# Optimization experiments

Hardware: AMD Instinct MI355X
Metric: run time of the kernel (lower is better)

## Reference

```python
import jax, jax.numpy as jnp
import numpy as np


def setup_inputs() -> dict:
    key = jax.random.key(0)
    ks = jax.random.split(key, 9)
    B, Chsi, Cmsi, Cout, H, W = 2, 128, 64, 128, 80, 80
    return {
        "z_hsi": jax.random.normal(ks[0], (B, Chsi, H, W), dtype=jnp.float32),
        "z_msi": jax.random.normal(ks[1], (B, Cmsi, H, W), dtype=jnp.float32),
        "Wq": jax.random.normal(ks[2], (Cout, Chsi), dtype=jnp.float32) * 0.05,
        "bq": jax.random.normal(ks[3], (Cout,), dtype=jnp.float32) * 0.05,
        "Wk": jax.random.normal(ks[4], (Cout, Cmsi), dtype=jnp.float32) * 0.05,
        "bk": jax.random.normal(ks[5], (Cout,), dtype=jnp.float32) * 0.05,
        "Wv": jax.random.normal(ks[6], (Cout, Cmsi), dtype=jnp.float32) * 0.05,
        "bv": jax.random.normal(ks[7], (Cout,), dtype=jnp.float32) * 0.05,
        "gamma": jax.random.normal(ks[8], (1,), dtype=jnp.float32),
    }


def reference(z_hsi, z_msi, Wq, bq, Wk, bk, Wv, bv, gamma):
    B, C, H, W = z_hsi.shape
    N = H * W
    # 1x1 convs are per-pixel channel mixes
    q = jnp.einsum('bchw,oc->bohw', z_hsi, Wq) + bq[None, :, None, None]  # (B,O,H,W)
    k = jnp.einsum('bchw,oc->bohw', z_msi, Wk) + bk[None, :, None, None]
    v = jnp.einsum('bchw,oc->bohw', z_msi, Wv) + bv[None, :, None, None]
    q = q.reshape(B, -1, N)  # (B,O,N)
    k = k.reshape(B, -1, N)
    v = v.reshape(B, -1, N)
    # energy[b,i,j] = sum_o q[b,o,i] * k[b,o,j]  (unscaled, as in source)
    energy = jnp.einsum('boi,boj->bij', q, k)  # (B,N,N)
    attn = jax.nn.softmax(energy, axis=-1)
    # out[b,o,i] = sum_j v[b,o,j] * attn[b,i,j]
    out = jnp.einsum('boj,bij->boi', v, attn).reshape(B, -1, H, W)
    return gamma * out + z_hsi
```

## Files before the change

### kernel.cpp

```cpp
#include <hip/hip_runtime.h>
#include <hip/hip_bf16.h>
#include <hip/hip_fp16.h>

#define B_    2
#define N_    6400
#define CD_   128
#define CM_   64
#define SEG_  5
#define JSEG_ (N_ / SEG_)
#define JT_   64
#define NJT_  (JSEG_ / JT_)
#define NIT_  50

typedef __attribute__((ext_vector_type(8)))  short bf16x8;
typedef __attribute__((ext_vector_type(16))) float f32x16;
typedef __attribute__((ext_vector_type(2)))  __fp16 f16x2;

static __device__ __forceinline__ unsigned pack2bf(float a, float b) {
    union { float f; unsigned u; } x, y; x.f = a; y.f = b;
    return __builtin_amdgcn_perm(y.u + 0x8000u, x.u + 0x8000u, 0x07060302u);
}

static __device__ __forceinline__ unsigned cvtpk_bf16(float a, float b) {
    unsigned r;
    asm("v_cvt_pk_bf16_f32 %0, %1, %2" : "=v"(r) : "v"(a), "v"(b));
    return r;
}

__global__ __launch_bounds__(256, 4)
void proj2(const float* __restrict__ zh, const float* __restrict__ zm,
           const float* __restrict__ Wq, const float* __restrict__ bq,
           const float* __restrict__ Wk, const float* __restrict__ bk,
           const float* __restrict__ Wv, const float* __restrict__ bv,
           short* __restrict__ qb, short* __restrict__ kb, short* __restrict__ vb)
{
    __shared__ float zt[128 * 68];
    const int tid = threadIdx.x;
    int bid = blockIdx.x;
    const int qmode = bid < 400;
    if (!qmode) bid -= 400;
    const int b  = bid / 200;
    const int r  = bid % 200;
    const int i0 = (r >> 1) * 64;
    const int o0 = (r & 1) * 64;
    const int ig = tid & 15, og = tid >> 4;
    const int il = ig * 4;

    if (qmode) {
        const float* zsrc = zh + (size_t)b * CD_ * N_ + i0;
#pragma unroll
        for (int rep = 0; rep < 8; ++rep) {
            int idx = tid + rep * 256;
            int c = idx >> 4, f = idx & 15;
            *(float4*)&zt[c * 68 + f * 4] = *(const float4*)&zsrc[(size_t)c * N_ + f * 4];
        }
        __syncthreads();
        const float* wr0 = Wq + (size_t)(o0 + og * 4 + 0) * CD_;
        const float* wr1 = Wq + (size_t)(o0 + og * 4 + 1) * CD_;
        const float* wr2 = Wq + (size_t)(o0 + og * 4 + 2) * CD_;
        const float* wr3 = Wq + (size_t)(o0 + og * 4 + 3) * CD_;
        float acc[4][4];
#pragma unroll
        for (int oi = 0; oi < 4; ++oi) {
            float bb = bq[o0 + og * 4 + oi];
#pragma unroll
            for (int ri = 0; ri < 4; ++ri) acc[ri][oi] = bb;
        }
        for (int c4 = 0; c4 < 32; ++c4) {
            float4 w0 = *(const float4*)&wr0[c4 * 4];
            float4 w1 = *(const float4*)&wr1[c4 * 4];
            float4 w2 = *(const float4*)&wr2[c4 * 4];
            float4 w3 = *(const float4*)&wr3[c4 * 4];
            float ww[4][4] = {{w0.x,w1.x,w2.x,w3.x},{w0.y,w1.y,w2.y,w3.y},
                              {w0.z,w1.z,w2.z,w3.z},{w0.w,w1.w,w2.w,w3.w}};
#pragma unroll
            for (int cc = 0; cc < 4; ++cc) {
                float4 zr = *(float4*)&zt[(c4 * 4 + cc) * 68 + il];
                float zz[4] = {zr.x, zr.y, zr.z, zr.w};
#pragma unroll
                for (int ri = 0; ri < 4; ++ri)
#pragma unroll
                    for (int oi = 0; oi < 4; ++oi)
                        acc[ri][oi] = fmaf(zz[ri], ww[cc][oi], acc[ri][oi]);
            }
        }
#pragma unroll
        for (int ri = 0; ri < 4; ++ri) {
            uint2 pk = make_uint2(pack2bf(acc[ri][0], acc[ri][1]),
                                  pack2bf(acc[ri][2], acc[ri][3]));
            *(uint2*)&qb[((size_t)b * N_ + i0 + il + ri) * CD_ + o0 + og * 4] = pk;
        }
    } else {
        const float* zsrc = zm + (size_t)b * CM_ * N_ + i0;
#pragma unroll
        for (int rep = 0; rep < 4; ++rep) {
            int idx = tid + rep * 256;
            int c = idx >> 4, f = idx & 15;
            *(float4*)&zt[c * 68 + f * 4] = *(const float4*)&zsrc[(size_t)c * N_ + f * 4];
        }
        __syncthreads();
        const float* kr0 = Wk + (size_t)(o0 + og * 4 + 0) * CM_;
        const float* kr1 = Wk + (size_t)(o0 + og * 4 + 1) * CM_;
        const float* kr2 = Wk + (size_t)(o0 + og * 4 + 2) * CM_;
        const float* kr3 = Wk + (size_t)(o0 + og * 4 + 3) * CM_;
        const float* vr0 = Wv + (size_t)(o0 + og * 4 + 0) * CM_;
        const float* vr1 = Wv + (size_t)(o0 + og * 4 + 1) * CM_;
        const float* vr2 = Wv + (size_t)(o0 + og * 4 + 2) * CM_;
        const float* vr3 = Wv + (size_t)(o0 + og * 4 + 3) * CM_;
        float ak[4][4], av[4][4];
#pragma unroll
        for (int oi = 0; oi < 4; ++oi) {
            float bk0 = bk[o0 + og * 4 + oi], bv0 = bv[o0 + og * 4 + oi];
#pragma unroll
            for (int ri = 0; ri < 4; ++ri) { ak[ri][oi] = bk0; av[ri][oi] = bv0; }
        }
        for (int c4 = 0; c4 < 16; ++c4) {
            float4 k0 = *(const float4*)&kr0[c4 * 4];
            float4 k1 = *(const float4*)&kr1[c4 * 4];
            float4 k2 = *(const float4*)&kr2[c4 * 4];
            float4 k3 = *(const float4*)&kr3[c4 * 4];
            float4 v0 = *(const float4*)&vr0[c4 * 4];
            float4 v1 = *(const float4*)&vr1[c4 * 4];
            float4 v2 = *(const float4*)&vr2[c4 * 4];
            float4 v3 = *(const float4*)&vr3[c4 * 4];
            float kk[4][4] = {{k0.x,k1.x,k2.x,k3.x},{k0.y,k1.y,k2.y,k3.y},
                              {k0.z,k1.z,k2.z,k3.z},{k0.w,k1.w,k2.w,k3.w}};
            float vv[4][4] = {{v0.x,v1.x,v2.x,v3.x},{v0.y,v1.y,v2.y,v3.y},
                              {v0.z,v1.z,v2.z,v3.z},{v0.w,v1.w,v2.w,v3.w}};
#pragma unroll
            for (int cc = 0; cc < 4; ++cc) {
                float4 zr = *(float4*)&zt[(c4 * 4 + cc) * 68 + il];
                float zz[4] = {zr.x, zr.y, zr.z, zr.w};
#pragma unroll
                for (int ri = 0; ri < 4; ++ri)
#pragma unroll
                    for (int oi = 0; oi < 4; ++oi) {
                        ak[ri][oi] = fmaf(zz[ri], kk[cc][oi], ak[ri][oi]);
                        av[ri][oi] = fmaf(zz[ri], vv[cc][oi], av[ri][oi]);
                    }
            }
        }
#pragma unroll
        for (int ri = 0; ri < 4; ++ri) {
            uint2 pk = make_uint2(pack2bf(ak[ri][0], ak[ri][1]),
                                  pack2bf(ak[ri][2], ak[ri][3]));
            *(uint2*)&kb[((size_t)b * N_ + i0 + il + ri) * CD_ + o0 + og * 4] = pk;
        }
        const size_t vbase = (size_t)b * CD_ * N_;
#pragma unroll
        for (int oi = 0; oi < 4; ++oi) {
            uint2 pk = make_uint2(pack2bf(av[0][oi], av[1][oi]),
                                  pack2bf(av[2][oi], av[3][oi]));
            *(uint2*)&vb[vbase + (size_t)(o0 + og * 4 + oi) * N_ + i0 + il] = pk;
        }
    }
}

__global__ __launch_bounds__(256, 2)
void flash6(const short* __restrict__ qb, const short* __restrict__ kb,
            const short* __restrict__ vb, __fp16* __restrict__ Op,
            float* __restrict__ ml)
{
    __shared__ short Ks[2][64 * 128];
    __shared__ short Vs[2][128 * 64];

    const int tid   = threadIdx.x;
    const int wid   = tid >> 6;
    const int lane  = tid & 63;
    const int m5    = lane & 31;
    const int h     = lane >> 5;
    const int m15   = m5 & 15;
    const int l4r   = lane >> 4;
    const int pc    = (lane & 15) ^ l4r;

    const int vrow = lane >> 3;
    const int vc8  = (lane & 7) ^ (vrow & 7);
    const int voff = vrow * (N_ * 2) + vc8 * 16;

    const int bid = blockIdx.x;
    const int s   = bid % SEG_;
    const int bIt = bid / SEG_;
    const int b   = bIt >= NIT_ ? 1 : 0;
    const int it  = bIt - b * NIT_;
    const int i0  = it * 128;
    const int jbase = s * JSEG_;

    const short* qbp = qb + (size_t)b * N_ * CD_;
    const short* kbp = kb + (size_t)b * N_ * CD_;
    const char*  vstage = (const char*)(vb + (size_t)b * CD_ * N_) + voff;

    const int irow = i0 + wid * 32 + m5;
    bf16x8 qf[8];
#pragma unroll
    for (int kw = 0; kw < 8; ++kw)
        qf[kw] = *(const bf16x8*)&qbp[(size_t)irow * CD_ + kw * 16 + h * 8];

    f32x16 acc[4];
#pragma unroll
    for (int os = 0; os < 4; ++os)
#pragma unroll
        for (int r2 = 0; r2 < 16; ++r2) acc[os][r2] = 0.f;
    float lrun = 0.f;

#pragma unroll
    for (int tt = 0; tt < 4; ++tt) {
        int t = wid * 4 + tt;
        int st = (4 * t) & 15;
        const char* g = (const char*)kbp + (size_t)(jbase + 4 * t + l4r) * 256
                        + ((pc ^ st) << 4);
        __builtin_amdgcn_global_load_lds(
            (const __attribute__((address_space(1))) void*)g,
            (__attribute__((address_space(3))) void*)&Ks[0][t * 512], 16, 0, 0);
    }
#pragma unroll
    for (int tt = 0; tt < 4; ++tt) {
        int t = wid * 4 + tt;
        const char* g = vstage + (size_t)(t * 8) * (N_ * 2) + (size_t)jbase * 2;
        __builtin_amdgcn_global_load_lds(
            (const __attribute__((address_space(1))) void*)g,
            (__attribute__((address_space(3))) void*)&Vs[0][t * 512], 16, 0, 0);
    }
    __syncthreads();

    for (int jti = 0; jti < NJT_; ++jti) {
        const int jt  = jbase + jti * JT_;
        const int cur = jti & 1;
        if (jti + 1 < NJT_) {
            const int jn = jt + JT_;
#pragma unroll
            for (int tt = 0; tt < 4; ++tt) {
                int t = wid * 4 + tt;
                int st = (4 * t) & 15;
                const char* g = (const char*)kbp + (size_t)(jn + 4 * t + l4r) * 256
                                + ((pc ^ st) << 4);
                __builtin_amdgcn_global_load_lds(
                    (const __attribute__((address_space(1))) void*)g,
                    (__attribute__((address_space(3))) void*)&Ks[1 - cur][t * 512], 16, 0, 0);
            }
#pragma unroll
            for (int tt = 0; tt < 4; ++tt) {
                int t = wid * 4 + tt;
                const char* g = vstage + (size_t)(t * 8) * (N_ * 2) + (size_t)jn * 2;
                __builtin_amdgcn_global_load_lds(
                    (const __attribute__((address_space(1))) void*)g,
                    (__attribute__((address_space(3))) void*)&Vs[1 - cur][t * 512], 16, 0, 0);
            }
        }

        unsigned fr[4][4];
#pragma unroll
        for (int jc = 0; jc < 2; ++jc) {
            f32x16 sacc;
#pragma unroll
            for (int r2 = 0; r2 < 16; ++r2) sacc[r2] = 0.f;
            __builtin_amdgcn_s_setprio(1);
#pragma unroll
            for (int kw = 0; kw < 8; ++kw) {
                int c16 = (2 * kw + h) ^ m15;
                bf16x8 kf = *(const bf16x8*)&Ks[cur][(jc * 32 + m5) * 128 + c16 * 8];
                sacc = __builtin_amdgcn_mfma_f32_32x32x16_bf16(kf, qf[kw], sacc, 0, 0, 0);
            }
            __builtin_amdgcn_s_setprio(0);
            unsigned pk[8];
#pragma unroll
            for (int p = 0; p < 8; ++p) {
                float e0 = __expf(sacc[2 * p]     - 25.f);
                float e1 = __expf(sacc[2 * p + 1] - 25.f);
                lrun += e0 + e1;
                pk[p] = cvtpk_bf16(e0, e1);
            }
#pragma unroll
            for (int X = 0; X < 2; ++X) {
                auto r0 = __builtin_amdgcn_permlane32_swap(
                              pk[4 * X],     pk[4 * X + 2], false, false);
                auto r1 = __builtin_amdgcn_permlane32_swap(
                              pk[4 * X + 1], pk[4 * X + 3], false, false);
                fr[2 * jc + X][0] = (unsigned)r0[0];
                fr[2 * jc + X][1] = (unsigned)r1[0];
                fr[2 * jc + X][2] = (unsigned)r0[1];
                fr[2 * jc + X][3] = (unsigned)r1[1];
            }
        }
        __builtin_amdgcn_s_setprio(1);
#pragma unroll
        for (int kc = 0; kc < 4; ++kc) {
            union { unsigned u[4]; bf16x8 v; } pf;
#pragma unroll
            for (int u = 0; u < 4; ++u) pf.u[u] = fr[kc][u];
#pragma unroll
            for (int os = 0; os < 4; ++os) {
                int o = os * 32 + m5;
                int q = (kc * 2 + h) ^ (m5 & 7);
                bf16x8 vf = *(const bf16x8*)&Vs[cur][o * 64 + q * 8];
                acc[os] = __builtin_amdgcn_mfma_f32_32x32x16_bf16(vf, pf.v, acc[os], 0, 0, 0);
            }
        }
        __builtin_amdgcn_s_setprio(0);
        __syncthreads();
    }

    float lt = lrun + __shfl_xor(lrun, 32);
    if (h == 0) ml[((size_t)bIt * SEG_ + s) * 128 + wid * 32 + m5] = lt;
    const float linv = 1.0f / lt;

    float* Of = (float*)&Ks[0][0];
    __fp16* opb = Op + ((size_t)bIt * SEG_ + s) * (128 * CD_);
#pragma unroll
    for (int r = 0; r < 2; ++r) {
        __syncthreads();
        if ((wid >> 1) == r) {
            const int il_ = (wid & 1) * 32 + m5;
#pragma unroll
            for (int os = 0; os < 4; ++os) {
#pragma unroll
                for (int g = 0; g < 4; ++g) {
                    int q = os * 8 + g * 2 + h;
                    int p = q ^ m5;
                    *(float4*)&Of[il_ * 128 + p * 4] =
                        make_float4(acc[os][4 * g] * linv, acc[os][4 * g + 1] * linv,
                                    acc[os][4 * g + 2] * linv, acc[os][4 * g + 3] * linv);
                }
            }
        }
        __syncthreads();
#pragma unroll
        for (int u = 0; u < 8; ++u) {
            int G = u * 256 + tid;
            int i = G >> 5;
            int q = tid & 31;
            int p = q ^ (i & 31);
            float4 t = *(float4*)&Of[i * 128 + p * 4];
            union { f16x2 h2[2]; uint2 u2; } cv;
            cv.h2[0] = __builtin_amdgcn_cvt_pkrtz(t.x, t.y);
            cv.h2[1] = __builtin_amdgcn_cvt_pkrtz(t.z, t.w);
            *(uint2*)&opb[(size_t)r * 64 * CD_ + (size_t)G * 4] = cv.u2;
        }
    }
}

__global__ __launch_bounds__(256, 4)
void combine3(const __fp16* __restrict__ Op, const float* __restrict__ ml,
              const float* __restrict__ z_hsi, const float* __restrict__ gamma,
              float* __restrict__ out)
{
    __shared__ float T[CD_ * 36];
    __shared__ float wbuf[SEG_][32];
    const int tid = threadIdx.x;
    const int blk = blockIdx.x;
    const int bIt = blk >> 2;
    const int rq  = (blk & 3) * 32;
    const int b   = bIt / NIT_;
    const int it  = bIt % NIT_;
    const int i0  = it * 128 + rq;
    const float g = gamma[0];

    if (tid < 32) {
        float l[SEG_];
        float den = 0.f;
#pragma unroll
        for (int s2 = 0; s2 < SEG_; ++s2) {
            l[s2] = ml[((size_t)bIt * SEG_ + s2) * 128 + rq + tid];
            den += l[s2];
        }
        const float gd = g / den;
#pragma unroll
        for (int s2 = 0; s2 < SEG_; ++s2)
            wbuf[s2][tid] = l[s2] * gd;
    }
    __syncthreads();
    {
        const int i  = tid >> 3;
        const int oc = (tid & 7) * 4;
        float w[SEG_];
#pragma unroll
        for (int s2 = 0; s2 < SEG_; ++s2) w[s2] = wbuf[s2][i];
        const __fp16* base = Op + ((size_t)bIt * SEG_ * 128 + rq + i) * CD_ + oc;
#pragma unroll
        for (int c4 = 0; c4 < 4; ++c4) {
            float ax = 0.f, ay = 0.f, az = 0.f, aw = 0.f;
#pragma unroll
            for (int s2 = 0; s2 < SEG_; ++s2) {
                union { uint2 u2; f16x2 h2[2]; } raw;
                raw.u2 = *(const uint2*)&base[(size_t)s2 * 128 * CD_ + c4 * 32];
                ax = fmaf((float)raw.h2[0][0], w[s2], ax);
                ay = fmaf((float)raw.h2[0][1], w[s2], ay);
                az = fmaf((float)raw.h2[1][0], w[s2], az);
                aw = fmaf((float)raw.h2[1][1], w[s2], aw);
            }
            int o = oc + c4 * 32;
            T[(o + 0) * 36 + i] = ax;
            T[(o + 1) * 36 + i] = ay;
            T[(o + 2) * 36 + i] = az;
            T[(o + 3) * 36 + i] = aw;
        }
    }
    __syncthreads();
    {
        const int o = tid >> 1, ih = (tid & 1) * 16;
        const size_t gbase = ((size_t)b * CD_ + o) * N_ + i0 + ih;
#pragma unroll
        for (int rr = 0; rr < 4; ++rr) {
            float4 t  = *(float4*)&T[o * 36 + ih + rr * 4];
            float4 z4 = *(const float4*)&z_hsi[gbase + rr * 4];
            *(float4*)&out[gbase + rr * 4] =
                make_float4(t.x + z4.x, t.y + z4.y, t.z + z4.z, t.w + z4.w);
        }
    }
}

extern "C" void kernel_launch(void* const* d_in, const int* in_sizes, int n_in,
                              void* d_out, int out_size, void* d_ws, size_t ws_size,
                              hipStream_t stream) {
    const float* z_hsi = (const float*)d_in[0];
    const float* z_msi = (const float*)d_in[1];
    const float* Wq    = (const float*)d_in[2];
    const float* bq    = (const float*)d_in[3];
    const float* Wk    = (const float*)d_in[4];
    const float* bk    = (const float*)d_in[5];
    const float* Wv    = (const float*)d_in[6];
    const float* bv    = (const float*)d_in[7];
    const float* gamma = (const float*)d_in[8];
    float* out = (float*)d_out;

    const size_t nqb = (size_t)B_ * N_ * CD_;
    short* qb = (short*)d_ws;
    short* kb = qb + nqb;
    short* vb = kb + nqb;
    __fp16* Op = (__fp16*)(vb + nqb);
    float* ml = (float*)(Op + (size_t)100 * SEG_ * 128 * CD_);

    proj2<<<dim3(800), dim3(256), 0, stream>>>(z_hsi, z_msi, Wq, bq, Wk, bk, Wv, bv,
                                               qb, kb, vb);
    flash6<<<dim3(100 * SEG_), dim3(256), 0, stream>>>(qb, kb, vb, Op, ml);
    combine3<<<dim3(400), dim3(256), 0, stream>>>(Op, ml, z_hsi, gamma, out);
}
```

Measured before the change: 155.5 us.

## Fuse projection, flash attention and combine into one persistent kernel with grid barriers

Merges the three kernels into one persistent kernel of 500 blocks. Grid-wide atomic barriers separate the projection, attention and combine phases, and the projection work is looped over the resident blocks. It also folds log2(e) into q so the softmax can use exp2f with a pre-biased accumulator instead of __expf with a subtraction. This removes two kernel launch gaps and the tail effects between them, but relies on all 500 blocks being co-resident and adds a memset plus spin-wait barrier cost.

```diff
diff --git a/kernel.cpp b/kernel.cpp
--- a/kernel.cpp
+++ b/kernel.cpp
@@ -11,6 +11,8 @@
 #define JT_   64
 #define NJT_  (JSEG_ / JT_)
 #define NIT_  50
+#define GRID_ (NIT_ * 2 * SEG_)
+#define LOG2E_ 1.4426950408889634f
 
 typedef __attribute__((ext_vector_type(8)))  short bf16x8;
 typedef __attribute__((ext_vector_type(16))) float f32x16;
@@ -27,383 +29,400 @@
     return r;
 }
 
-__global__ __launch_bounds__(256, 4)
-void proj2(const float* __restrict__ zh, const float* __restrict__ zm,
+static __device__ __forceinline__ void gridbar(unsigned* bar) {
+    __syncthreads();
+    __threadfence();
+    if (threadIdx.x == 0) {
+        __hip_atomic_fetch_add(bar, 1u, __ATOMIC_RELEASE, __HIP_MEMORY_SCOPE_AGENT);
+        while (__hip_atomic_load(bar, __ATOMIC_ACQUIRE, __HIP_MEMORY_SCOPE_AGENT) < GRID_)
+            __builtin_amdgcn_s_sleep(1);
+    }
+    __syncthreads();
+    __threadfence();
+}
+
+__global__ __launch_bounds__(256, 2)
+void fused(const float* __restrict__ zh, const float* __restrict__ zm,
            const float* __restrict__ Wq, const float* __restrict__ bq,
            const float* __restrict__ Wk, const float* __restrict__ bk,
            const float* __restrict__ Wv, const float* __restrict__ bv,
-           short* __restrict__ qb, short* __restrict__ kb, short* __restrict__ vb)
+           short* __restrict__ qb, short* __restrict__ kb, short* __restrict__ vb,
+           __fp16* __restrict__ Op, float* __restrict__ ml,
+           const float* __restrict__ gamma, float* __restrict__ out,
+           unsigned* __restrict__ bar)
 {
-    __shared__ float zt[128 * 68];
+    __shared__ __align__(16) char smem[65536];
     const int tid = threadIdx.x;
-    int bid = blockIdx.x;
-    const int qmode = bid < 400;
-    if (!qmode) bid -= 400;
-    const int b  = bid / 200;
-    const int r  = bid % 200;
-    const int i0 = (r >> 1) * 64;
-    const int o0 = (r & 1) * 64;
-    const int ig = tid & 15, og = tid >> 4;
-    const int il = ig * 4;
-
-    if (qmode) {
-        const float* zsrc = zh + (size_t)b * CD_ * N_ + i0;
-#pragma unroll
-        for (int rep = 0; rep < 8; ++rep) {
-            int idx = tid + rep * 256;
-            int c = idx >> 4, f = idx & 15;
-            *(float4*)&zt[c * 68 + f * 4] = *(const float4*)&zsrc[(size_t)c * N_ + f * 4];
+
+    {
+        float* zt = (float*)smem;
+        const int ig = tid & 15, og = tid >> 4;
+        const int il = ig * 4;
+        for (int u = blockIdx.x; u < 800; u += GRID_) {
+            int ub = u;
+            const int qmode = ub < 400;
+            if (!qmode) ub -= 400;
+            const int b  = ub / 200;
+            const int r  = ub % 200;
+            const int i0 = (r >> 1) * 64;
+            const int o0 = (r & 1) * 64;
+
+            if (qmode) {
+                const float* zsrc = zh + (size_t)b * CD_ * N_ + i0;
+#pragma unroll
+                for (int rep = 0; rep < 8; ++rep) {
+                    int idx = tid + rep * 256;
+                    int c = idx >> 4, f = idx & 15;
+                    *(float4*)&zt[c * 68 + f * 4] = *(const float4*)&zsrc[(size_t)c * N_ + f * 4];
+                }
+                __syncthreads();
+                const float* wr0 = Wq + (size_t)(o0 + og * 4 + 0) * CD_;
+                const float* wr1 = Wq + (size_t)(o0 + og * 4 + 1) * CD_;
+                const float* wr2 = Wq + (size_t)(o0 + og * 4 + 2) * CD_;
+                const float* wr3 = Wq + (size_t)(o0 + og * 4 + 3) * CD_;
+                float acc[4][4];
+#pragma unroll
+                for (int oi = 0; oi < 4; ++oi) {
+                    float bb = bq[o0 + og * 4 + oi];
+#pragma unroll
+                    for (int ri = 0; ri < 4; ++ri) acc[ri][oi] = bb;
+                }
+                for (int c4 = 0; c4 < 32; ++c4) {
+                    float4 w0 = *(const float4*)&wr0[c4 * 4];
+                    float4 w1 = *(const float4*)&wr1[c4 * 4];
+                    float4 w2 = *(const float4*)&wr2[c4 * 4];
+                    float4 w3 = *(const float4*)&wr3[c4 * 4];
+                    float ww[4][4] = {{w0.x,w1.x,w2.x,w3.x},{w0.y,w1.y,w2.y,w3.y},
+                                      {w0.z,w1.z,w2.z,w3.z},{w0.w,w1.w,w2.w,w3.w}};
+#pragma unroll
+                    for (int cc = 0; cc < 4; ++cc) {
+                        float4 zr = *(float4*)&zt[(c4 * 4 + cc) * 68 + il];
+                        float zz[4] = {zr.x, zr.y, zr.z, zr.w};
+#pragma unroll
+                        for (int ri = 0; ri < 4; ++ri)
+#pragma unroll
+                            for (int oi = 0; oi < 4; ++oi)
+                                acc[ri][oi] = fmaf(zz[ri], ww[cc][oi], acc[ri][oi]);
+                    }
+                }
+#pragma unroll
+                for (int ri = 0; ri < 4; ++ri) {
+                    uint2 pk = make_uint2(
+                        pack2bf(acc[ri][0] * LOG2E_, acc[ri][1] * LOG2E_),
+                        pack2bf(acc[ri][2] * LOG2E_, acc[ri][3] * LOG2E_));
+                    *(uint2*)&qb[((size_t)b * N_ + i0 + il + ri) * CD_ + o0 + og * 4] = pk;
+                }
+            } else {
+                const float* zsrc = zm + (size_t)b * CM_ * N_ + i0;
+#pragma unroll
+                for (int rep = 0; rep < 4; ++rep) {
+                    int idx = tid + rep * 256;
+                    int c = idx >> 4, f = idx & 15;
+                    *(float4*)&zt[c * 68 + f * 4] = *(const float4*)&zsrc[(size_t)c * N_ + f * 4];
+                }
+                __syncthreads();
+                const float* kr0 = Wk + (size_t)(o0 + og * 4 + 0) * CM_;
+                const float* kr1 = Wk + (size_t)(o0 + og * 4 + 1) * CM_;
+                const float* kr2 = Wk + (size_t)(o0 + og * 4 + 2) * CM_;
+                const float* kr3 = Wk + (size_t)(o0 + og * 4 + 3) * CM_;
+                const float* vr0 = Wv + (size_t)(o0 + og * 4 + 0) * CM_;
+                const float* vr1 = Wv + (size_t)(o0 + og * 4 + 1) * CM_;
+                const float* vr2 = Wv + (size_t)(o0 + og * 4 + 2) * CM_;
+                const float* vr3 = Wv + (size_t)(o0 + og * 4 + 3) * CM_;
+                float ak[4][4], av[4][4];
+#pragma unroll
+                for (int oi = 0; oi < 4; ++oi) {
+                    float bk0 = bk[o0 + og * 4 + oi], bv0 = bv[o0 + og * 4 + oi];
+#pragma unroll
+                    for (int ri = 0; ri < 4; ++ri) { ak[ri][oi] = bk0; av[ri][oi] = bv0; }
+                }
+                for (int c4 = 0; c4 < 16; ++c4) {
+                    float4 k0 = *(const float4*)&kr0[c4 * 4];
+                    float4 k1 = *(const float4*)&kr1[c4 * 4];
+                    float4 k2 = *(const float4*)&kr2[c4 * 4];
+                    float4 k3 = *(const float4*)&kr3[c4 * 4];
+                    float4 v0 = *(const float4*)&vr0[c4 * 4];
+                    float4 v1 = *(const float4*)&vr1[c4 * 4];
+                    float4 v2 = *(const float4*)&vr2[c4 * 4];
+                    float4 v3 = *(const float4*)&vr3[c4 * 4];
+                    float kk[4][4] = {{k0.x,k1.x,k2.x,k3.x},{k0.y,k1.y,k2.y,k3.y},
+                                      {k0.z,k1.z,k2.z,k3.z},{k0.w,k1.w,k2.w,k3.w}};
+                    float vv[4][4] = {{v0.x,v1.x,v2.x,v3.x},{v0.y,v1.y,v2.y,v3.y},
+                                      {v0.z,v1.z,v2.z,v3.z},{v0.w,v1.w,v2.w,v3.w}};
+#pragma unroll
+                    for (int cc = 0; cc < 4; ++cc) {
+                        float4 zr = *(float4*)&zt[(c4 * 4 + cc) * 68 + il];
+                        float zz[4] = {zr.x, zr.y, zr.z, zr.w};
+#pragma unroll
+                        for (int ri = 0; ri < 4; ++ri)
+#pragma unroll
+                            for (int oi = 0; oi < 4; ++oi) {
+                                ak[ri][oi] = fmaf(zz[ri], kk[cc][oi], ak[ri][oi]);
+                                av[ri][oi] = fmaf(zz[ri], vv[cc][oi], av[ri][oi]);
+                            }
+                    }
+                }
+#pragma unroll
+                for (int ri = 0; ri < 4; ++ri) {
+                    uint2 pk = make_uint2(pack2bf(ak[ri][0], ak[ri][1]),
+                                          pack2bf(ak[ri][2], ak[ri][3]));
+                    *(uint2*)&kb[((size_t)b * N_ + i0 + il + ri) * CD_ + o0 + og * 4] = pk;
+                }
+                const size_t vbase = (size_t)b * CD_ * N_;
+#pragma unroll
+                for (int oi = 0; oi < 4; ++oi) {
+                    uint2 pk = make_uint2(pack2bf(av[0][oi], av[1][oi]),
+                                          pack2bf(av[2][oi], av[3][oi]));
+                    *(uint2*)&vb[vbase + (size_t)(o0 + og * 4 + oi) * N_ + i0 + il] = pk;
+                }
+            }
+            __syncthreads();
+        }
+    }
+
+    gridbar(&bar[0]);
+
+    {
+        short* Ks0 = (short*)smem;
+        short* Vs0 = (short*)(smem + 32768);
+
+        const int wid   = tid >> 6;
+        const int lane  = tid & 63;
+        const int m5    = lane & 31;
+        const int h     = lane >> 5;
+        const int m15   = m5 & 15;
+        const int l4r   = lane >> 4;
+        const int pc    = (lane & 15) ^ l4r;
+
+        const int vrow = lane >> 3;
+        const int vc8  = (lane & 7) ^ (vrow & 7);
+        const int voff = vrow * (N_ * 2) + vc8 * 16;
+
+        const int bid = blockIdx.x;
+        const int s   = bid % SEG_;
+        const int bIt = bid / SEG_;
+        const int b   = bIt >= NIT_ ? 1 : 0;
+        const int it  = bIt - b * NIT_;
+        const int i0  = it * 128;
+        const int jbase = s * JSEG_;
+
+        const short* qbp = qb + (size_t)b * N_ * CD_;
+        const short* kbp = kb + (size_t)b * N_ * CD_;
+        const char*  vstage = (const char*)(vb + (size_t)b * CD_ * N_) + voff;
+
+        const int irow = i0 + wid * 32 + m5;
+        bf16x8 qf[8];
+#pragma unroll
+        for (int kw = 0; kw < 8; ++kw)
+            qf[kw] = *(const bf16x8*)&qbp[(size_t)irow * CD_ + kw * 16 + h * 8];
+
+        f32x16 acc[4];
+#pragma unroll
+        for (int os = 0; os < 4; ++os)
+#pragma unroll
+            for (int r2 = 0; r2 < 16; ++r2) acc[os][r2] = 0.f;
+        float lrun = 0.f;
+
+#pragma unroll
+        for (int tt = 0; tt < 4; ++tt) {
+            int t = wid * 4 + tt;
+            int st = (4 * t) & 15;
+            const char* g = (const char*)kbp + (size_t)(jbase + 4 * t + l4r) * 256
+                            + ((pc ^ st) << 4);
+            __builtin_amdgcn_global_load_lds(
+                (const __attribute__((address_space(1))) void*)g,
+                (__attribute__((address_space(3))) void*)(Ks0 + t * 512), 16, 0, 0);
+        }
+#pragma unroll
+        for (int tt = 0; tt < 4; ++tt) {
+            int t = wid * 4 + tt;
+            const char* g = vstage + (size_t)(t * 8) * (N_ * 2) + (size_t)jbase * 2;
+            __builtin_amdgcn_global_load_lds(
+                (const __attribute__((address_space(1))) void*)g,
+                (__attribute__((address_space(3))) void*)(Vs0 + t * 512), 16, 0, 0);
         }
         __syncthreads();
-        const float* wr0 = Wq + (size_t)(o0 + og * 4 + 0) * CD_;
-        const float* wr1 = Wq + (size_t)(o0 + og * 4 + 1) * CD_;
-        const float* wr2 = Wq + (size_t)(o0 + og * 4 + 2) * CD_;
-        const float* wr3 = Wq + (size_t)(o0 + og * 4 + 3) * CD_;
-        float acc[4][4];
-#pragma unroll
-        for (int oi = 0; oi < 4; ++oi) {
-            float bb = bq[o0 + og * 4 + oi];
-#pragma unroll
-            for (int ri = 0; ri < 4; ++ri) acc[ri][oi] = bb;
-        }
-        for (int c4 = 0; c4 < 32; ++c4) {
-            float4 w0 = *(const float4*)&wr0[c4 * 4];
-            float4 w1 = *(const float4*)&wr1[c4 * 4];
-            float4 w2 = *(const float4*)&wr2[c4 * 4];
-            float4 w3 = *(const float4*)&wr3[c4 * 4];
-            float ww[4][4] = {{w0.x,w1.x,w2.x,w3.x},{w0.y,w1.y,w2.y,w3.y},
-                              {w0.z,w1.z,w2.z,w3.z},{w0.w,w1.w,w2.w,w3.w}};
-#pragma unroll
-            for (int cc = 0; cc < 4; ++cc) {
-                float4 zr = *(float4*)&zt[(c4 * 4 + cc) * 68 + il];
-                float zz[4] = {zr.x, zr.y, zr.z, zr.w};
-#pragma unroll
-                for (int ri = 0; ri < 4; ++ri)
-#pragma unroll
-                    for (int oi = 0; oi < 4; ++oi)
-                        acc[ri][oi] = fmaf(zz[ri], ww[cc][oi], acc[ri][oi]);
-            }
-        }
-#pragma unroll
-        for (int ri = 0; ri < 4; ++ri) {
-            uint2 pk = make_uint2(pack2bf(acc[ri][0], acc[ri][1]),
-                                  pack2bf(acc[ri][2], acc[ri][3]));
-            *(uint2*)&qb[((size_t)b * N_ + i0 + il + ri) * CD_ + o0 + og * 4] = pk;
-        }
-    } else {
-        const float* zsrc = zm + (size_t)b * CM_ * N_ + i0;
-#pragma unroll
-        for (int rep = 0; rep < 4; ++rep) {
-            int idx = tid + rep * 256;
-            int c = idx >> 4, f = idx & 15;
-            *(float4*)&zt[c * 68 + f * 4] = *(const float4*)&zsrc[(size_t)c * N_ + f * 4];
+
+        for (int jti = 0; jti < NJT_; ++jti) {
+            const int jt  = jbase + jti * JT_;
+            const int cur = jti & 1;
+            if (jti + 1 < NJT_) {
+                const int jn = jt + JT_;
+#pragma unroll
+                for (int tt = 0; tt < 4; ++tt) {
+                    int t = wid * 4 + tt;
+                    int st = (4 * t) & 15;
+                    const char* g = (const char*)kbp + (size_t)(jn + 4 * t + l4r) * 256
+                                    + ((pc ^ st) << 4);
+                    __builtin_amdgcn_global_load_lds(
+                        (const __attribute__((address_space(1))) void*)g,
+                        (__attribute__((address_space(3))) void*)(Ks0 + (1 - cur) * 8192 + t * 512), 16, 0, 0);
+                }
+#pragma unroll
+                for (int tt = 0; tt < 4; ++tt) {
+                    int t = wid * 4 + tt;
+                    const char* g = vstage + (size_t)(t * 8) * (N_ * 2) + (size_t)jn * 2;
+                    __builtin_amdgcn_global_load_lds(
+                        (const __attribute__((address_space(1))) void*)g,
+                        (__attribute__((address_space(3))) void*)(Vs0 + (1 - cur) * 8192 + t * 512), 16, 0, 0);
+                }
+            }
+
+            unsigned fr[4][4];
+#pragma unroll
+            for (int jc = 0; jc < 2; ++jc) {
+                f32x16 sacc;
+#pragma unroll
+                for (int r2 = 0; r2 < 16; ++r2) sacc[r2] = -36.067376022224085f;
+                __builtin_amdgcn_s_setprio(1);
+#pragma unroll
+                for (int kw = 0; kw < 8; ++kw) {
+                    int c16 = (2 * kw + h) ^ m15;
+                    bf16x8 kf = *(const bf16x8*)&Ks0[cur * 8192 + (jc * 32 + m5) * 128 + c16 * 8];
+                    sacc = __builtin_amdgcn_mfma_f32_32x32x16_bf16(kf, qf[kw], sacc, 0, 0, 0);
+                }
+                __builtin_amdgcn_s_setprio(0);
+                unsigned pk[8];
+#pragma unroll
+                for (int p = 0; p < 8; ++p) {
+                    float e0 = exp2f(sacc[2 * p]);
+                    float e1 = exp2f(sacc[2 * p + 1]);
+                    lrun += e0 + e1;
+                    pk[p] = cvtpk_bf16(e0, e1);
+                }
+#pragma unroll
+                for (int X = 0; X < 2; ++X) {
+                    auto r0 = __builtin_amdgcn_permlane32_swap(
+                                  pk[4 * X],     pk[4 * X + 2], false, false);
+                    auto r1 = __builtin_amdgcn_permlane32_swap(
+                                  pk[4 * X + 1], pk[4 * X + 3], false, false);
+                    fr[2 * jc + X][0] = (unsigned)r0[0];
+                    fr[2 * jc + X][1] = (unsigned)r1[0];
+                    fr[2 * jc + X][2] = (unsigned)r0[1];
+                    fr[2 * jc + X][3] = (unsigned)r1[1];
+                }
+            }
+            __builtin_amdgcn_s_setprio(1);
+#pragma unroll
+            for (int kc = 0; kc < 4; ++kc) {
+                union { unsigned u[4]; bf16x8 v; } pf;
+#pragma unroll
+                for (int u = 0; u < 4; ++u) pf.u[u] = fr[kc][u];
+#pragma unroll
+                for (int os = 0; os < 4; ++os) {
+                    int o = os * 32 + m5;
+                    int q = (kc * 2 + h) ^ (m5 & 7);
+                    bf16x8 vf = *(const bf16x8*)&Vs0[cur * 8192 + o * 64 + q * 8];
+                    acc[os] = __builtin_amdgcn_mfma_f32_32x32x16_bf16(vf, pf.v, acc[os], 0, 0, 0);
+                }
+            }
+            __builtin_amdgcn_s_setprio(0);
+            __syncthreads();
+        }
+
+        float lt = lrun + __shfl_xor(lrun, 32);
+        if (h == 0) ml[((size_t)bIt * SEG_ + s) * 128 + wid * 32 + m5] = lt;
+        const float linv = 1.0f / lt;
+
+        float* Of = (float*)smem;
+        __fp16* opb = Op + ((size_t)bIt * SEG_ + s) * (128 * CD_);
+#pragma unroll
+        for (int r = 0; r < 2; ++r) {
+            __syncthreads();
+            if ((wid >> 1) == r) {
+                const int il_ = (wid & 1) * 32 + m5;
+#pragma unroll
+                for (int os = 0; os < 4; ++os) {
+#pragma unroll
+                    for (int g = 0; g < 4; ++g) {
+                        int q = os * 8 + g * 2 + h;
+                        int p = q ^ m5;
+                        *(float4*)&Of[il_ * 128 + p * 4] =
+                            make_float4(acc[os][4 * g] * linv, acc[os][4 * g + 1] * linv,
+                                        acc[os][4 * g + 2] * linv, acc[os][4 * g + 3] * linv);
+                    }
+                }
+            }
+            __syncthreads();
+#pragma unroll
+            for (int u = 0; u < 8; ++u) {
+                int G = u * 256 + tid;
+                int i = G >> 5;
+                int q = tid & 31;
+                int p = q ^ (i & 31);
+                float4 t = *(float4*)&Of[i * 128 + p * 4];
+                union { f16x2 h2[2]; uint2 u2; } cv;
+                cv.h2[0] = __builtin_amdgcn_cvt_pkrtz(t.x, t.y);
+                cv.h2[1] = __builtin_amdgcn_cvt_pkrtz(t.z, t.w);
+                *(uint2*)&opb[(size_t)r * 64 * CD_ + (size_t)G * 4] = cv.u2;
+            }
+        }
+    }
+
+    gridbar(&bar[1]);
+
+    if (blockIdx.x < 400) {
+        float* T = (float*)smem;
+        float (*wbuf)[32] = (float(*)[32])(smem + 18944);
+        const int blk = blockIdx.x;
+        const int bIt = blk >> 2;
+        const int rq  = (blk & 3) * 32;
+        const int b   = bIt / NIT_;
+        const int it  = bIt % NIT_;
+        const int i0  = it * 128 + rq;
+        const float g = gamma[0];
+
+        if (tid < 32) {
+            float l[SEG_];
+            float den = 0.f;
+#pragma unroll
+            for (int s2 = 0; s2 < SEG_; ++s2) {
+                l[s2] = ml[((size_t)bIt * SEG_ + s2) * 128 + rq + tid];
+                den += l[s2];
+            }
+            const float gd = g / den;
+#pragma unroll
+            for (int s2 = 0; s2 < SEG_; ++s2)
+                wbuf[s2][tid] = l[s2] * gd;
         }
         __syncthreads();
-        const float* kr0 = Wk + (size_t)(o0 + og * 4 + 0) * CM_;
-        const float* kr1 = Wk + (size_t)(o0 + og * 4 + 1) * CM_;
-        const float* kr2 = Wk + (size_t)(o0 + og * 4 + 2) * CM_;
-        const float* kr3 = Wk + (size_t)(o0 + og * 4 + 3) * CM_;
-        const float* vr0 = Wv + (size_t)(o0 + og * 4 + 0) * CM_;
-        const float* vr1 = Wv + (size_t)(o0 + og * 4 + 1) * CM_;
-        const float* vr2 = Wv + (size_t)(o0 + og * 4 + 2) * CM_;
-        const float* vr3 = Wv + (size_t)(o0 + og * 4 + 3) * CM_;
-        float ak[4][4], av[4][4];
-#pragma unroll
-        for (int oi = 0; oi < 4; ++oi) {
-            float bk0 = bk[o0 + og * 4 + oi], bv0 = bv[o0 + og * 4 + oi];
-#pragma unroll
-            for (int ri = 0; ri < 4; ++ri) { ak[ri][oi] = bk0; av[ri][oi] = bv0; }
-        }
-        for (int c4 = 0; c4 < 16; ++c4) {
-            float4 k0 = *(const float4*)&kr0[c4 * 4];
-            float4 k1 = *(const float4*)&kr1[c4 * 4];
-            float4 k2 = *(const float4*)&kr2[c4 * 4];
-            float4 k3 = *(const float4*)&kr3[c4 * 4];
-            float4 v0 = *(const float4*)&vr0[c4 * 4];
-            float4 v1 = *(const float4*)&vr1[c4 * 4];
-            float4 v2 = *(const float4*)&vr2[c4 * 4];
-            float4 v3 = *(const float4*)&vr3[c4 * 4];
-            float kk[4][4] = {{k0.x,k1.x,k2.x,k3.x},{k0.y,k1.y,k2.y,k3.y},
-                              {k0.z,k1.z,k2.z,k3.z},{k0.w,k1.w,k2.w,k3.w}};
-            float vv[4][4] = {{v0.x,v1.x,v2.x,v3.x},{v0.y,v1.y,v2.y,v3.y},
-                              {v0.z,v1.z,v2.z,v3.z},{v0.w,v1.w,v2.w,v3.w}};
-#pragma unroll
-            for (int cc = 0; cc < 4; ++cc) {
-                float4 zr = *(float4*)&zt[(c4 * 4 + cc) * 68 + il];
-                float zz[4] = {zr.x, zr.y, zr.z, zr.w};
-#pragma unroll
-                for (int ri = 0; ri < 4; ++ri)
-#pragma unroll
-                    for (int oi = 0; oi < 4; ++oi) {
-                        ak[ri][oi] = fmaf(zz[ri], kk[cc][oi], ak[ri][oi]);
-                        av[ri][oi] = fmaf(zz[ri], vv[cc][oi], av[ri][oi]);
-                    }
-            }
-        }
-#pragma unroll
-        for (int ri = 0; ri < 4; ++ri) {
-            uint2 pk = make_uint2(pack2bf(ak[ri][0], ak[ri][1]),
-                                  pack2bf(ak[ri][2], ak[ri][3]));
-            *(uint2*)&kb[((size_t)b * N_ + i0 + il + ri) * CD_ + o0 + og * 4] = pk;
-        }
-        const size_t vbase = (size_t)b * CD_ * N_;
-#pragma unroll
-        for (int oi = 0; oi < 4; ++oi) {
-            uint2 pk = make_uint2(pack2bf(av[0][oi], av[1][oi]),
-                                  pack2bf(av[2][oi], av[3][oi]));
-            *(uint2*)&vb[vbase + (size_t)(o0 + og * 4 + oi) * N_ + i0 + il] = pk;
-        }
-    }
-}
-
-__global__ __launch_bounds__(256, 2)
-void flash6(const short* __restrict__ qb, const short* __restrict__ kb,
-            const short* __restrict__ vb, __fp16* __restrict__ Op,
-            float* __restrict__ ml)
-{
-    __shared__ short Ks[2][64 * 128];
-    __shared__ short Vs[2][128 * 64];
-
-    const int tid   = threadIdx.x;
-    const int wid   = tid >> 6;
-    const int lane  = tid & 63;
-    const int m5    = lane & 31;
-    const int h     = lane >> 5;
-    const int m15   = m5 & 15;
-    const int l4r   = lane >> 4;
-    const int pc    = (lane & 15) ^ l4r;
-
-    const int vrow = lane >> 3;
-    const int vc8  = (lane & 7) ^ (vrow & 7);
-    const int voff = vrow * (N_ * 2) + vc8 * 16;
-
-    const int bid = blockIdx.x;
-    const int s   = bid % SEG_;
-    const int bIt = bid / SEG_;
-    const int b   = bIt >= NIT_ ? 1 : 0;
-    const int it  = bIt - b * NIT_;
-    const int i0  = it * 128;
-    const int jbase = s * JSEG_;
-
-    const short* qbp = qb + (size_t)b * N_ * CD_;
-    const short* kbp = kb + (size_t)b * N_ * CD_;
-    const char*  vstage = (const char*)(vb + (size_t)b * CD_ * N_) + voff;
-
-    const int irow = i0 + wid * 32 + m5;
-    bf16x8 qf[8];
-#pragma unroll
-    for (int kw = 0; kw < 8; ++kw)
-        qf[kw] = *(const bf16x8*)&qbp[(size_t)irow * CD_ + kw * 16 + h * 8];
-
-    f32x16 acc[4];
-#pragma unroll
-    for (int os = 0; os < 4; ++os)
-#pragma unroll
-        for (int r2 = 0; r2 < 16; ++r2) acc[os][r2] = 0.f;
-    float lrun = 0.f;
-
-#pragma unroll
-    for (int tt = 0; tt < 4; ++tt) {
-        int t = wid * 4 + tt;
-        int st = (4 * t) & 15;
-        const char* g = (const char*)kbp + (size_t)(jbase + 4 * t + l4r) * 256
-                        + ((pc ^ st) << 4);
-        __builtin_amdgcn_global_load_lds(
-            (const __attribute__((address_space(1))) void*)g,
-            (__attribute__((address_space(3))) void*)&Ks[0][t * 512], 16, 0, 0);
-    }
-#pragma unroll
-    for (int tt = 0; tt < 4; ++tt) {
-        int t = wid * 4 + tt;
-        const char* g = vstage + (size_t)(t * 8) * (N_ * 2) + (size_t)jbase * 2;
-        __builtin_amdgcn_global_load_lds(
-            (const __attribute__((address_space(1))) void*)g,
-            (__attribute__((address_space(3))) void*)&Vs[0][t * 512], 16, 0, 0);
-    }
-    __syncthreads();
-
-    for (int jti = 0; jti < NJT_; ++jti) {
-        const int jt  = jbase + jti * JT_;
-        const int cur = jti & 1;
-        if (jti + 1 < NJT_) {
-            const int jn = jt + JT_;
-#pragma unroll
-            for (int tt = 0; tt < 4; ++tt) {
-                int t = wid * 4 + tt;
-                int st = (4 * t) & 15;
-                const char* g = (const char*)kbp + (size_t)(jn + 4 * t + l4r) * 256
-                                + ((pc ^ st) << 4);
-                __builtin_amdgcn_global_load_lds(
-                    (const __attribute__((address_space(1))) void*)g,
-                    (__attribute__((address_space(3))) void*)&Ks[1 - cur][t * 512], 16, 0, 0);
-            }
-#pragma unroll
-            for (int tt = 0; tt < 4; ++tt) {
-                int t = wid * 4 + tt;
-                const char* g = vstage + (size_t)(t * 8) * (N_ * 2) + (size_t)jn * 2;
-                __builtin_amdgcn_global_load_lds(
-                    (const __attribute__((address_space(1))) void*)g,
-                    (__attribute__((address_space(3))) void*)&Vs[1 - cur][t * 512], 16, 0, 0);
-            }
-        }
-
-        unsigned fr[4][4];
-#pragma unroll
-        for (int jc = 0; jc < 2; ++jc) {
-            f32x16 sacc;
-#pragma unroll
-            for (int r2 = 0; r2 < 16; ++r2) sacc[r2] = 0.f;
-            __builtin_amdgcn_s_setprio(1);
-#pragma unroll
-            for (int kw = 0; kw < 8; ++kw) {
-                int c16 = (2 * kw + h) ^ m15;
-                bf16x8 kf = *(const bf16x8*)&Ks[cur][(jc * 32 + m5) * 128 + c16 * 8];
-                sacc = __builtin_amdgcn_mfma_f32_32x32x16_bf16(kf, qf[kw], sacc, 0, 0, 0);
-            }
-            __builtin_amdgcn_s_setprio(0);
-            unsigned pk[8];
-#pragma unroll
-            for (int p = 0; p < 8; ++p) {
-                float e0 = __expf(sacc[2 * p]     - 25.f);
-                float e1 = __expf(sacc[2 * p + 1] - 25.f);
-                lrun += e0 + e1;
-                pk[p] = cvtpk_bf16(e0, e1);
-            }
-#pragma unroll
-            for (int X = 0; X < 2; ++X) {
-                auto r0 = __builtin_amdgcn_permlane32_swap(
-                              pk[4 * X],     pk[4 * X + 2], false, false);
-                auto r1 = __builtin_amdgcn_permlane32_swap(
-                              pk[4 * X + 1], pk[4 * X + 3], false, false);
-                fr[2 * jc + X][0] = (unsigned)r0[0];
-                fr[2 * jc + X][1] = (unsigned)r1[0];
-                fr[2 * jc + X][2] = (unsigned)r0[1];
-                fr[2 * jc + X][3] = (unsigned)r1[1];
-            }
-        }
-        __builtin_amdgcn_s_setprio(1);
-#pragma unroll
-        for (int kc = 0; kc < 4; ++kc) {
-            union { unsigned u[4]; bf16x8 v; } pf;
-#pragma unroll
-            for (int u = 0; u < 4; ++u) pf.u[u] = fr[kc][u];
-#pragma unroll
-            for (int os = 0; os < 4; ++os) {
-                int o = os * 32 + m5;
-                int q = (kc * 2 + h) ^ (m5 & 7);
-                bf16x8 vf = *(const bf16x8*)&Vs[cur][o * 64 + q * 8];
-                acc[os] = __builtin_amdgcn_mfma_f32_32x32x16_bf16(vf, pf.v, acc[os], 0, 0, 0);
-            }
-        }
-        __builtin_amdgcn_s_setprio(0);
+        {
+            const int i  = tid >> 3;
+            const int oc = (tid & 7) * 4;
+            float w[SEG_];
+#pragma unroll
+            for (int s2 = 0; s2 < SEG_; ++s2) w[s2] = wbuf[s2][i];
+            const __fp16* base = Op + ((size_t)bIt * SEG_ * 128 + rq + i) * CD_ + oc;
+#pragma unroll
+            for (int c4 = 0; c4 < 4; ++c4) {
+                float ax = 0.f, ay = 0.f, az = 0.f, aw = 0.f;
+#pragma unroll
+                for (int s2 = 0; s2 < SEG_; ++s2) {
+                    union { uint2 u2; f16x2 h2[2]; } raw;
+                    raw.u2 = *(const uint2*)&base[(size_t)s2 * 128 * CD_ + c4 * 32];
+                    ax = fmaf((float)raw.h2[0][0], w[s2], ax);
+                    ay = fmaf((float)raw.h2[0][1], w[s2], ay);
+                    az = fmaf((float)raw.h2[1][0], w[s2], az);
+                    aw = fmaf((float)raw.h2[1][1], w[s2], aw);
+                }
+                int o = oc + c4 * 32;
+                T[(o + 0) * 36 + i] = ax;
+                T[(o + 1) * 36 + i] = ay;
+                T[(o + 2) * 36 + i] = az;
+                T[(o + 3) * 36 + i] = aw;
+            }
+        }
         __syncthreads();
-    }
-
-    float lt = lrun + __shfl_xor(lrun, 32);
-    if (h == 0) ml[((size_t)bIt * SEG_ + s) * 128 + wid * 32 + m5] = lt;
-    const float linv = 1.0f / lt;
-
-    float* Of = (float*)&Ks[0][0];
-    __fp16* opb = Op + ((size_t)bIt * SEG_ + s) * (128 * CD_);
-#pragma unroll
-    for (int r = 0; r < 2; ++r) {
-        __syncthreads();
-        if ((wid >> 1) == r) {
-            const int il_ = (wid & 1) * 32 + m5;
-#pragma unroll
-            for (int os = 0; os < 4; ++os) {
-#pragma unroll
-                for (int g = 0; g < 4; ++g) {
-                    int q = os * 8 + g * 2 + h;
-                    int p = q ^ m5;
-                    *(float4*)&Of[il_ * 128 + p * 4] =
-                        make_float4(acc[os][4 * g] * linv, acc[os][4 * g + 1] * linv,
-                                    acc[os][4 * g + 2] * linv, acc[os][4 * g + 3] * linv);
-                }
-            }
-        }
-        __syncthreads();
-#pragma unroll
-        for (int u = 0; u < 8; ++u) {
-            int G = u * 256 + tid;
-            int i = G >> 5;
-            int q = tid & 31;
-            int p = q ^ (i & 31);
-            float4 t = *(float4*)&Of[i * 128 + p * 4];
-            union { f16x2 h2[2]; uint2 u2; } cv;
-            cv.h2[0] = __builtin_amdgcn_cvt_pkrtz(t.x, t.y);
-            cv.h2[1] = __builtin_amdgcn_cvt_pkrtz(t.z, t.w);
-            *(uint2*)&opb[(size_t)r * 64 * CD_ + (size_t)G * 4] = cv.u2;
-        }
-    }
-}
-
-__global__ __launch_bounds__(256, 4)
-void combine3(const __fp16* __restrict__ Op, const float* __restrict__ ml,
-              const float* __restrict__ z_hsi, const float* __restrict__ gamma,
-              float* __restrict__ out)
-{
-    __shared__ float T[CD_ * 36];
-    __shared__ float wbuf[SEG_][32];
-    const int tid = threadIdx.x;
-    const int blk = blockIdx.x;
-    const int bIt = blk >> 2;
-    const int rq  = (blk & 3) * 32;
-    const int b   = bIt / NIT_;
-    const int it  = bIt % NIT_;
-    const int i0  = it * 128 + rq;
-    const float g = gamma[0];
-
-    if (tid < 32) {
-        float l[SEG_];
-        float den = 0.f;
-#pragma unroll
-        for (int s2 = 0; s2 < SEG_; ++s2) {
-            l[s2] = ml[((size_t)bIt * SEG_ + s2) * 128 + rq + tid];
-            den += l[s2];
-        }
-        const float gd = g / den;
-#pragma unroll
-        for (int s2 = 0; s2 < SEG_; ++s2)
-            wbuf[s2][tid] = l[s2] * gd;
-    }
-    __syncthreads();
-    {
-        const int i  = tid >> 3;
-        const int oc = (tid & 7) * 4;
-        float w[SEG_];
-#pragma unroll
-        for (int s2 = 0; s2 < SEG_; ++s2) w[s2] = wbuf[s2][i];
-        const __fp16* base = Op + ((size_t)bIt * SEG_ * 128 + rq + i) * CD_ + oc;
-#pragma unroll
-        for (int c4 = 0; c4 < 4; ++c4) {
-            float ax = 0.f, ay = 0.f, az = 0.f, aw = 0.f;
-#pragma unroll
-            for (int s2 = 0; s2 < SEG_; ++s2) {
-                union { uint2 u2; f16x2 h2[2]; } raw;
-                raw.u2 = *(const uint2*)&base[(size_t)s2 * 128 * CD_ + c4 * 32];
-                ax = fmaf((float)raw.h2[0][0], w[s2], ax);
-                ay = fmaf((float)raw.h2[0][1], w[s2], ay);
-                az = fmaf((float)raw.h2[1][0], w[s2], az);
-                aw = fmaf((float)raw.h2[1][1], w[s2], aw);
-            }
-            int o = oc + c4 * 32;
-            T[(o + 0) * 36 + i] = ax;
-            T[(o + 1) * 36 + i] = ay;
-            T[(o + 2) * 36 + i] = az;
-            T[(o + 3) * 36 + i] = aw;
-        }
-    }
-    __syncthreads();
-    {
-        const int o = tid >> 1, ih = (tid & 1) * 16;
-        const size_t gbase = ((size_t)b * CD_ + o) * N_ + i0 + ih;
-#pragma unroll
-        for (int rr = 0; rr < 4; ++rr) {
-            float4 t  = *(float4*)&T[o * 36 + ih + rr * 4];
-            float4 z4 = *(const float4*)&z_hsi[gbase + rr * 4];
-            *(float4*)&out[gbase + rr * 4] =
-                make_float4(t.x + z4.x, t.y + z4.y, t.z + z4.z, t.w + z4.w);
+        {
+            const int o = tid >> 1, ih = (tid & 1) * 16;
+            const size_t gbase = ((size_t)b * CD_ + o) * N_ + i0 + ih;
+#pragma unroll
+            for (int rr = 0; rr < 4; ++rr) {
+                float4 t  = *(float4*)&T[o * 36 + ih + rr * 4];
+                float4 z4 = *(const float4*)&zh[gbase + rr * 4];
+                *(float4*)&out[gbase + rr * 4] =
+                    make_float4(t.x + z4.x, t.y + z4.y, t.z + z4.z, t.w + z4.w);
+            }
         }
     }
 }
@@ -428,9 +447,10 @@
     short* vb = kb + nqb;
     __fp16* Op = (__fp16*)(vb + nqb);
     float* ml = (float*)(Op + (size_t)100 * SEG_ * 128 * CD_);
-
-    proj2<<<dim3(800), dim3(256), 0, stream>>>(z_hsi, z_msi, Wq, bq, Wk, bk, Wv, bv,
-                                               qb, kb, vb);
-    flash6<<<dim3(100 * SEG_), dim3(256), 0, stream>>>(qb, kb, vb, Op, ml);
-    combine3<<<dim3(400), dim3(256), 0, stream>>>(Op, ml, z_hsi, gamma, out);
+    unsigned* bar = (unsigned*)(ml + (size_t)100 * SEG_ * 128);
+
+    hipMemsetAsync(bar, 0, 2 * sizeof(unsigned), stream);
+    fused<<<dim3(GRID_), dim3(256), 0, stream>>>(
+        z_hsi, z_msi, Wq, bq, Wk, bk, Wv, bv,
+        qb, kb, vb, Op, ml, gamma, out, bar);
 }
```

Result: slower. 474.8 us (+205.4%).
